# Performance work log

Hardware: AMD Instinct MI355X
Metric: run time of the kernel (lower is better)

Reference implementation:

```python
import jax, jax.numpy as jnp
import numpy as np

N_NODES = 100000
N_EDGES = 1600000
D_FEAT = 48
K = 2


def setup_inputs() -> dict:
    key = jax.random.key(0)
    k1, k2, k3, k4 = jax.random.split(key, 4)
    x = jax.random.normal(k1, (N_NODES, D_FEAT), dtype=jnp.float32)
    edge_weight = jax.random.uniform(k2, (N_EDGES,), dtype=jnp.float32)
    edge_src = jax.random.randint(k3, (N_EDGES,), 0, N_NODES, dtype=jnp.int32)
    edge_dst = jax.random.randint(k4, (N_EDGES,), 0, N_NODES, dtype=jnp.int32)
    return {"x": x, "edge_weight": edge_weight, "edge_src": edge_src, "edge_dst": edge_dst}


def _spmm(edge_weight, edge_src, edge_dst, x):
    # out[i] = sum_{e: dst[e]==i} w[e] * x[src[e]]   (sparse adj @ x)
    msgs = edge_weight[:, None] * x[edge_src]  # [E, F]
    return jax.ops.segment_sum(msgs, edge_dst, num_segments=N_NODES)


def reference(x, edge_weight, edge_src, edge_dst):
    for _ in range(K):
        x = _spmm(edge_weight, edge_src, edge_dst, x)
    return x
```

## Files before the change

kernel.cpp:

```cpp
#include <hip/hip_runtime.h>

#define N_NODES 100000
#define N_EDGES 1600000
#define D_FEAT  48

#define BKT_SHIFT 9
#define BKT_NODES (1 << BKT_SHIFT)
#define NBKT ((N_NODES + BKT_NODES - 1) / BKT_NODES)
#define EPB1 2048
#define NB1  ((N_EDGES + EPB1 - 1) / EPB1)

__device__ __forceinline__ unsigned short bf16_rn(float f) {
    unsigned u = __float_as_uint(f);
    unsigned r = (u + 0x7fffu + ((u >> 16) & 1u)) >> 16;
    return (unsigned short)r;
}
__device__ __forceinline__ float bf2f(unsigned short b) {
    return __uint_as_float(((unsigned)b) << 16);
}

__global__ void cvt_bf16_kernel(const float* __restrict__ in,
                                unsigned short* __restrict__ outb, int n4) {
    int i = blockIdx.x * blockDim.x + threadIdx.x;
    int stride = gridDim.x * blockDim.x;
    const float4* in4 = (const float4*)in;
    ushort4* o4 = (ushort4*)outb;
    for (; i < n4; i += stride) {
        float4 v = in4[i];
        ushort4 o;
        o.x = bf16_rn(v.x); o.y = bf16_rn(v.y);
        o.z = bf16_rn(v.z); o.w = bf16_rn(v.w);
        o4[i] = o;
    }
}


__global__ void hist1_kernel(const int* __restrict__ dst, int* __restrict__ ccount) {
    __shared__ int cnt[NBKT];
    for (int i = threadIdx.x; i < NBKT; i += blockDim.x) cnt[i] = 0;
    __syncthreads();
    int stride = gridDim.x * blockDim.x;
    for (int e = blockIdx.x * blockDim.x + threadIdx.x; e < N_EDGES; e += stride)
        atomicAdd(&cnt[dst[e] >> BKT_SHIFT], 1);
    __syncthreads();
    for (int i = threadIdx.x; i < NBKT; i += blockDim.x)
        if (cnt[i]) atomicAdd(&ccount[i], cnt[i]);
}

__global__ void scan196_kernel(const int* __restrict__ ccount,
                               int* __restrict__ bbase,
                               int* __restrict__ cursor,
                               int* __restrict__ row_ptr) {
    __shared__ int sdata[256];
    int t = threadIdx.x;
    int v = (t < NBKT) ? ccount[t] : 0;
    sdata[t] = v;
    __syncthreads();
    for (int off = 1; off < 256; off <<= 1) {
        int u = (t >= off) ? sdata[t - off] : 0;
        __syncthreads();
        sdata[t] += u;
        __syncthreads();
    }
    if (t < NBKT) { int ex = sdata[t] - v; bbase[t] = ex; cursor[t] = ex; }
    if (t == 0)   { bbase[NBKT] = N_EDGES; row_ptr[N_NODES] = N_EDGES; }
}

__global__ void p1_kernel(const float* __restrict__ w,
                          const int*   __restrict__ src,
                          const int*   __restrict__ dst,
                          int*         __restrict__ cursor,
                          uint2*       __restrict__ coarse) {
    __shared__ uint2 stage[EPB1];
    __shared__ unsigned char sbkt[EPB1];
    __shared__ int cnt[NBKT], base[NBKT];
    for (int i = threadIdx.x; i < NBKT; i += blockDim.x) cnt[i] = 0;
    __syncthreads();
    int e0 = blockIdx.x * EPB1;
    int n = N_EDGES - e0; if (n > EPB1) n = EPB1;
    for (int i = threadIdx.x; i < n; i += blockDim.x) {
        int e = e0 + i;
        int d = dst[e];
        int b = d >> BKT_SHIFT;
        atomicAdd(&cnt[b], 1);
        stage[i] = make_uint2((unsigned)(d & (BKT_NODES - 1)) | ((unsigned)src[e] << BKT_SHIFT),
                              (unsigned)__float_as_uint(w[e]));
        sbkt[i] = (unsigned char)b;
    }
    __syncthreads();
    for (int i = threadIdx.x; i < NBKT; i += blockDim.x) {
        int c = cnt[i];
        base[i] = c ? atomicAdd(&cursor[i], c) : 0;
        cnt[i] = 0;
    }
    __syncthreads();
    for (int i = threadIdx.x; i < n; i += blockDim.x) {
        int b = sbkt[i];
        int pos = base[b] + atomicAdd(&cnt[b], 1);
        coarse[pos] = stage[i];
    }
}

__global__ void p2_kernel(const uint2* __restrict__ coarse,
                          const int*   __restrict__ bbase,
                          int2*        __restrict__ recs,
                          int*         __restrict__ row_ptr) {
    __shared__ int cnt[BKT_NODES];
    __shared__ int ssum[256];
    int b = blockIdx.x, t = threadIdx.x;
    int lo = bbase[b], hi = bbase[b + 1];
    cnt[2 * t] = 0; cnt[2 * t + 1] = 0;
    __syncthreads();
    for (int i = lo + t; i < hi; i += 256)
        atomicAdd(&cnt[coarse[i].x & (BKT_NODES - 1)], 1);
    __syncthreads();
    int c0 = cnt[2 * t], c1 = cnt[2 * t + 1];
    int s = c0 + c1;
    ssum[t] = s;
    __syncthreads();
    for (int off = 1; off < 256; off <<= 1) {
        int u = (t >= off) ? ssum[t - off] : 0;
        __syncthreads();
        ssum[t] += u;
        __syncthreads();
    }
    int pre = lo + ssum[t] - s;
    int node0 = (b << BKT_SHIFT);
    cnt[2 * t] = pre;
    cnt[2 * t + 1] = pre + c0;
    if (node0 + 2 * t     < N_NODES) row_ptr[node0 + 2 * t]     = pre;
    if (node0 + 2 * t + 1 < N_NODES) row_ptr[node0 + 2 * t + 1] = pre + c0;
    __syncthreads();
    for (int i = lo + t; i < hi; i += 256) {
        uint2 r = coarse[i];
        int pos = atomicAdd(&cnt[r.x & (BKT_NODES - 1)], 1);
        recs[pos] = make_int2((int)(r.x >> BKT_SHIFT), (int)r.y);
    }
}

__device__ __forceinline__ void acc4(float* a, ushort4 u, float w) {
    a[0] += w * bf2f(u.x);
    a[1] += w * bf2f(u.y);
    a[2] += w * bf2f(u.z);
    a[3] += w * bf2f(u.w);
}

template <bool OUT_BF16>
__global__ void spmm_gather_b_kernel(const unsigned short* __restrict__ xb,
                                     const int2* __restrict__ recs,
                                     const int*  __restrict__ row_ptr,
                                     void* __restrict__ outv) {
    int tid = blockIdx.x * blockDim.x + threadIdx.x;
    int n = tid >> 2;
    int l = tid & 3;
    if (n >= N_NODES) return;
    int e   = row_ptr[n];
    int end = row_ptr[n + 1];
    float a0[4] = {0.f, 0.f, 0.f, 0.f};
    float a1[4] = {0.f, 0.f, 0.f, 0.f};
    float a2[4] = {0.f, 0.f, 0.f, 0.f};
    const ushort4* __restrict__ X = reinterpret_cast<const ushort4*>(xb);
    for (; e + 1 < end; e += 2) {
        int2 r0 = recs[e];
        int2 r1 = recs[e + 1];
        float w0 = __int_as_float(r0.y);
        float w1 = __int_as_float(r1.y);
        const ushort4* x0 = X + (size_t)r0.x * (D_FEAT / 4);
        const ushort4* x1 = X + (size_t)r1.x * (D_FEAT / 4);
        ushort4 u00 = x0[l], u01 = x0[4 + l], u02 = x0[8 + l];
        ushort4 u10 = x1[l], u11 = x1[4 + l], u12 = x1[8 + l];
        acc4(a0, u00, w0); acc4(a1, u01, w0); acc4(a2, u02, w0);
        acc4(a0, u10, w1); acc4(a1, u11, w1); acc4(a2, u12, w1);
    }
    if (e < end) {
        int2 r = recs[e];
        float we = __int_as_float(r.y);
        const ushort4* xr = X + (size_t)r.x * (D_FEAT / 4);
        acc4(a0, xr[l], we); acc4(a1, xr[4 + l], we); acc4(a2, xr[8 + l], we);
    }
    if (OUT_BF16) {
        ushort4* orow = reinterpret_cast<ushort4*>((unsigned short*)outv + (size_t)n * D_FEAT);
        ushort4 o0, o1, o2;
        o0.x = bf16_rn(a0[0]); o0.y = bf16_rn(a0[1]); o0.z = bf16_rn(a0[2]); o0.w = bf16_rn(a0[3]);
        o1.x = bf16_rn(a1[0]); o1.y = bf16_rn(a1[1]); o1.z = bf16_rn(a1[2]); o1.w = bf16_rn(a1[3]);
        o2.x = bf16_rn(a2[0]); o2.y = bf16_rn(a2[1]); o2.z = bf16_rn(a2[2]); o2.w = bf16_rn(a2[3]);
        orow[l] = o0; orow[4 + l] = o1; orow[8 + l] = o2;
    } else {
        float4* orow = reinterpret_cast<float4*>((float*)outv + (size_t)n * D_FEAT);
        orow[l]     = make_float4(a0[0], a0[1], a0[2], a0[3]);
        orow[4 + l] = make_float4(a1[0], a1[1], a1[2], a1[3]);
        orow[8 + l] = make_float4(a2[0], a2[1], a2[2], a2[3]);
    }
}

extern "C" void kernel_launch(void* const* d_in, const int* in_sizes, int n_in,
                              void* d_out, int out_size, void* d_ws, size_t ws_size,
                              hipStream_t stream) {
    const float* x    = (const float*)d_in[0];
    const float* ew   = (const float*)d_in[1];
    const int*   esrc = (const int*)d_in[2];
    const int*   edst = (const int*)d_in[3];
    float* out = (float*)d_out;

    char* ws = (char*)d_ws;
    unsigned short* xb = (unsigned short*)ws;
    ws += (((size_t)N_NODES * D_FEAT * sizeof(unsigned short)) + 15) & ~15ull;
    unsigned short* tmpb = (unsigned short*)ws;
    uint2* coarse = (uint2*)ws;
    ws += (size_t)N_EDGES * sizeof(uint2);
    int2* recs = (int2*)ws;
    ws += (size_t)N_EDGES * sizeof(int2);
    int* row_ptr = (int*)ws;
    ws += ((size_t)(N_NODES + 1) * sizeof(int) + 15) & ~15ull;
    int* ccount = (int*)ws;
    ws += ((size_t)NBKT * sizeof(int) + 15) & ~15ull;
    int* bbase = (int*)ws;
    ws += ((size_t)(NBKT + 1) * sizeof(int) + 15) & ~15ull;
    int* cursor = (int*)ws;

    dim3 blk(256);
    dim3 grid_nodes(((size_t)N_NODES * 4 + 255) / 256);

    hipMemsetAsync(ccount, 0, NBKT * sizeof(int), stream);
    cvt_bf16_kernel<<<1024, blk, 0, stream>>>(x, xb, (N_NODES * D_FEAT) / 4);
    hist1_kernel<<<1024, blk, 0, stream>>>(edst, ccount);
    scan196_kernel<<<1, blk, 0, stream>>>(ccount, bbase, cursor, row_ptr);
    p1_kernel<<<NB1, blk, 0, stream>>>(ew, esrc, edst, cursor, coarse);
    p2_kernel<<<NBKT, blk, 0, stream>>>(coarse, bbase, recs, row_ptr);

    spmm_gather_b_kernel<true><<<grid_nodes, blk, 0, stream>>>(xb, recs, row_ptr, tmpb);
    spmm_gather_b_kernel<false><<<grid_nodes, blk, 0, stream>>>(tmpb, recs, row_ptr, out);
}
```

Before: 258.7 us.

## Fuse bf16 convert with histogram, stage p2 edges in LDS, unroll gather by four

Merges the bf16 conversion and the bucket histogram into a single kernel, removing one launch. p2 now runs 512 threads per bucket and stages up to 9216 coarse edges in shared memory, so the second pass reads from LDS rather than global memory; edges beyond that cap still fall back to global reads. The SpMM gather loop is unrolled to four edges per iteration to keep more independent loads in flight. The cost is a large LDS footprint (about 72KB) in p2, which limits occupancy, plus higher register pressure in the gather.

```diff
diff --git a/kernel.cpp b/kernel.cpp
--- a/kernel.cpp
+++ b/kernel.cpp
@@ -9,6 +9,7 @@
 #define NBKT ((N_NODES + BKT_NODES - 1) / BKT_NODES)
 #define EPB1 2048
 #define NB1  ((N_EDGES + EPB1 - 1) / EPB1)
+#define P2_CAP 9216
 
 __device__ __forceinline__ unsigned short bf16_rn(float f) {
     unsigned u = __float_as_uint(f);
@@ -19,28 +20,26 @@
     return __uint_as_float(((unsigned)b) << 16);
 }
 
-__global__ void cvt_bf16_kernel(const float* __restrict__ in,
-                                unsigned short* __restrict__ outb, int n4) {
-    int i = blockIdx.x * blockDim.x + threadIdx.x;
+__global__ void cvt_hist_kernel(const float* __restrict__ in,
+                                unsigned short* __restrict__ outb,
+                                const int* __restrict__ dst,
+                                int* __restrict__ ccount) {
+    __shared__ int cnt[NBKT];
+    for (int i = threadIdx.x; i < NBKT; i += blockDim.x) cnt[i] = 0;
+    __syncthreads();
+    int tid = blockIdx.x * blockDim.x + threadIdx.x;
     int stride = gridDim.x * blockDim.x;
     const float4* in4 = (const float4*)in;
     ushort4* o4 = (ushort4*)outb;
-    for (; i < n4; i += stride) {
+    const int n4 = (N_NODES * D_FEAT) / 4;
+    for (int i = tid; i < n4; i += stride) {
         float4 v = in4[i];
         ushort4 o;
         o.x = bf16_rn(v.x); o.y = bf16_rn(v.y);
         o.z = bf16_rn(v.z); o.w = bf16_rn(v.w);
         o4[i] = o;
     }
-}
-
-
-__global__ void hist1_kernel(const int* __restrict__ dst, int* __restrict__ ccount) {
-    __shared__ int cnt[NBKT];
-    for (int i = threadIdx.x; i < NBKT; i += blockDim.x) cnt[i] = 0;
-    __syncthreads();
-    int stride = gridDim.x * blockDim.x;
-    for (int e = blockIdx.x * blockDim.x + threadIdx.x; e < N_EDGES; e += stride)
+    for (int e = tid; e < N_EDGES; e += stride)
         atomicAdd(&cnt[dst[e] >> BKT_SHIFT], 1);
     __syncthreads();
     for (int i = threadIdx.x; i < NBKT; i += blockDim.x)
@@ -101,38 +100,41 @@
     }
 }
 
-__global__ void p2_kernel(const uint2* __restrict__ coarse,
-                          const int*   __restrict__ bbase,
-                          int2*        __restrict__ recs,
-                          int*         __restrict__ row_ptr) {
+__global__ __launch_bounds__(512) void p2_kernel(const uint2* __restrict__ coarse,
+                                                 const int*   __restrict__ bbase,
+                                                 int2*        __restrict__ recs,
+                                                 int*         __restrict__ row_ptr) {
+    __shared__ uint2 sedge[P2_CAP];
     __shared__ int cnt[BKT_NODES];
-    __shared__ int ssum[256];
+    __shared__ int ssum[512];
     int b = blockIdx.x, t = threadIdx.x;
     int lo = bbase[b], hi = bbase[b + 1];
-    cnt[2 * t] = 0; cnt[2 * t + 1] = 0;
-    __syncthreads();
-    for (int i = lo + t; i < hi; i += 256)
-        atomicAdd(&cnt[coarse[i].x & (BKT_NODES - 1)], 1);
-    __syncthreads();
-    int c0 = cnt[2 * t], c1 = cnt[2 * t + 1];
-    int s = c0 + c1;
-    ssum[t] = s;
-    __syncthreads();
-    for (int off = 1; off < 256; off <<= 1) {
+    int m = hi - lo;
+    int staged = (m < P2_CAP) ? m : P2_CAP;
+    for (int i = t; i < staged; i += 512) sedge[i] = coarse[lo + i];
+    cnt[t] = 0;
+    __syncthreads();
+    for (int i = t; i < m; i += 512) {
+        uint2 r = (i < staged) ? sedge[i] : coarse[lo + i];
+        atomicAdd(&cnt[r.x & (BKT_NODES - 1)], 1);
+    }
+    __syncthreads();
+    int c = cnt[t];
+    ssum[t] = c;
+    __syncthreads();
+    for (int off = 1; off < 512; off <<= 1) {
         int u = (t >= off) ? ssum[t - off] : 0;
         __syncthreads();
         ssum[t] += u;
         __syncthreads();
     }
-    int pre = lo + ssum[t] - s;
-    int node0 = (b << BKT_SHIFT);
-    cnt[2 * t] = pre;
-    cnt[2 * t + 1] = pre + c0;
-    if (node0 + 2 * t     < N_NODES) row_ptr[node0 + 2 * t]     = pre;
-    if (node0 + 2 * t + 1 < N_NODES) row_ptr[node0 + 2 * t + 1] = pre + c0;
-    __syncthreads();
-    for (int i = lo + t; i < hi; i += 256) {
-        uint2 r = coarse[i];
+    int pre = lo + ssum[t] - c;
+    int node = (b << BKT_SHIFT) + t;
+    if (node < N_NODES) row_ptr[node] = pre;
+    cnt[t] = pre;
+    __syncthreads();
+    for (int i = t; i < m; i += 512) {
+        uint2 r = (i < staged) ? sedge[i] : coarse[lo + i];
         int pos = atomicAdd(&cnt[r.x & (BKT_NODES - 1)], 1);
         recs[pos] = make_int2((int)(r.x >> BKT_SHIFT), (int)r.y);
     }
@@ -160,19 +162,25 @@
     float a1[4] = {0.f, 0.f, 0.f, 0.f};
     float a2[4] = {0.f, 0.f, 0.f, 0.f};
     const ushort4* __restrict__ X = reinterpret_cast<const ushort4*>(xb);
-    for (; e + 1 < end; e += 2) {
-        int2 r0 = recs[e];
-        int2 r1 = recs[e + 1];
-        float w0 = __int_as_float(r0.y);
-        float w1 = __int_as_float(r1.y);
+    for (; e + 3 < end; e += 4) {
+        int2 r0 = recs[e],     r1 = recs[e + 1];
+        int2 r2 = recs[e + 2], r3 = recs[e + 3];
         const ushort4* x0 = X + (size_t)r0.x * (D_FEAT / 4);
         const ushort4* x1 = X + (size_t)r1.x * (D_FEAT / 4);
+        const ushort4* x2 = X + (size_t)r2.x * (D_FEAT / 4);
+        const ushort4* x3 = X + (size_t)r3.x * (D_FEAT / 4);
         ushort4 u00 = x0[l], u01 = x0[4 + l], u02 = x0[8 + l];
         ushort4 u10 = x1[l], u11 = x1[4 + l], u12 = x1[8 + l];
+        ushort4 u20 = x2[l], u21 = x2[4 + l], u22 = x2[8 + l];
+        ushort4 u30 = x3[l], u31 = x3[4 + l], u32 = x3[8 + l];
+        float w0 = __int_as_float(r0.y), w1 = __int_as_float(r1.y);
+        float w2 = __int_as_float(r2.y), w3 = __int_as_float(r3.y);
         acc4(a0, u00, w0); acc4(a1, u01, w0); acc4(a2, u02, w0);
         acc4(a0, u10, w1); acc4(a1, u11, w1); acc4(a2, u12, w1);
-    }
-    if (e < end) {
+        acc4(a0, u20, w2); acc4(a1, u21, w2); acc4(a2, u22, w2);
+        acc4(a0, u30, w3); acc4(a1, u31, w3); acc4(a2, u32, w3);
+    }
+    for (; e < end; ++e) {
         int2 r = recs[e];
         float we = __int_as_float(r.y);
         const ushort4* xr = X + (size_t)r.x * (D_FEAT / 4);
@@ -222,11 +230,10 @@
     dim3 grid_nodes(((size_t)N_NODES * 4 + 255) / 256);
 
     hipMemsetAsync(ccount, 0, NBKT * sizeof(int), stream);
-    cvt_bf16_kernel<<<1024, blk, 0, stream>>>(x, xb, (N_NODES * D_FEAT) / 4);
-    hist1_kernel<<<1024, blk, 0, stream>>>(edst, ccount);
+    cvt_hist_kernel<<<1024, blk, 0, stream>>>(x, xb, edst, ccount);
     scan196_kernel<<<1, blk, 0, stream>>>(ccount, bbase, cursor, row_ptr);
     p1_kernel<<<NB1, blk, 0, stream>>>(ew, esrc, edst, cursor, coarse);
-    p2_kernel<<<NBKT, blk, 0, stream>>>(coarse, bbase, recs, row_ptr);
+    p2_kernel<<<NBKT, dim3(512), 0, stream>>>(coarse, bbase, recs, row_ptr);
 
     spmm_gather_b_kernel<true><<<grid_nodes, blk, 0, stream>>>(xb, recs, row_ptr, tmpb);
     spmm_gather_b_kernel<false><<<grid_nodes, blk, 0, stream>>>(tmpb, recs, row_ptr, out);
```

Result: faster. 244.8 us (-5.4%).
